# Kernel optimization log

Measured on AMD Instinct MI355X. Metric: run time of the kernel, lower is better.

The kernel has to match this reference:

```python
import jax, jax.numpy as jnp
import numpy as np
from jax import lax

B, T, S = 32, 64, 400
H, E, EMB, V = 512, 1024, 256, 32000


def setup_inputs() -> dict:
    key = jax.random.key(0)
    ks = jax.random.split(key, 16)
    w = lambda k, shape: jax.random.normal(k, shape, dtype=jnp.float32) * 0.05
    return {
        "target": jax.random.randint(ks[0], (B, T), 0, V),
        "h0": jax.random.normal(ks[1], (B, H), dtype=jnp.float32),
        "c0": jax.random.normal(ks[2], (B, H), dtype=jnp.float32),
        "enc_outs": jax.random.normal(ks[3], (S, B, E), dtype=jnp.float32),
        "attn_mask": jnp.ones((B, S), dtype=jnp.int32),
        "emb": w(ks[4], (V, EMB)),
        "W_ih": w(ks[5], (4 * H, EMB)),
        "b_ih": w(ks[6], (4 * H,)),
        "W_hh": w(ks[7], (4 * H, H)),
        "b_hh": w(ks[8], (4 * H,)),
        "W_attn": w(ks[9], (H, E)),
        "b_attn": w(ks[10], (H,)),
        "W_concat": w(ks[11], (H, E + H)),
        "b_concat": w(ks[12], (H,)),
        "W_out": w(ks[13], (V, H)),
        "b_out": w(ks[14], (V,)),
    }


def reference(target, h0, c0, enc_outs, attn_mask, emb, W_ih, b_ih, W_hh, b_hh,
              W_attn, b_attn, W_concat, b_concat, W_out, b_out):
    # Precompute attention keys projection once: [S, B, H]
    keys_proj = jnp.einsum("sbe,he->sbh", enc_outs, W_attn) + b_attn
    masked = attn_mask == 0  # [B, S]
    x_seq = emb[target].transpose(1, 0, 2)  # [T, B, EMB]

    def step(carry, x_t):
        h, c = carry
        # LSTMCell (torch gate order: i, f, g, o)
        gates = x_t @ W_ih.T + b_ih + h @ W_hh.T + b_hh  # [B, 4H]
        i, f, g, o = jnp.split(gates, 4, axis=1)
        c = jax.nn.sigmoid(f) * c + jax.nn.sigmoid(i) * jnp.tanh(g)
        h = jax.nn.sigmoid(o) * jnp.tanh(c)
        # additive-style attention: sum over hidden of query*key_proj
        scores = jnp.einsum("bh,sbh->bs", h, keys_proj)  # [B, S]
        scores = jnp.where(masked, jnp.float32(-1e18), scores)
        a = jax.nn.softmax(scores, axis=1)
        ctx = jnp.einsum("bs,sbe->be", a, enc_outs)  # [B, E]
        cat = jnp.tanh(jnp.concatenate([ctx, h], axis=1) @ W_concat.T + b_concat)
        logit = jax.nn.log_softmax(cat @ W_out.T + b_out, axis=-1)  # [B, V]
        return (h, c), logit

    (_, _), logits = lax.scan(step, (h0, c0), x_seq)  # [T, B, V]
    return logits.transpose(1, 0, 2)  # [B, T, V]
```

## Files before the change

### kernel.cpp

```cpp
#include <hip/hip_runtime.h>
#include <hip/hip_bf16.h>
#include <hip/hip_fp16.h>

#define B_ 32
#define T_ 64
#define S_ 400
#define SPAD_ 512
#define H_ 512
#define E_ 1024
#define EMB_ 256
#define V_ 32000

typedef _Float16 f16;
typedef _Float16 half8 __attribute__((ext_vector_type(8)));
typedef float f32x4 __attribute__((ext_vector_type(4)));
typedef float f32x16 __attribute__((ext_vector_type(16)));
typedef unsigned uint4v __attribute__((ext_vector_type(4)));

__device__ __forceinline__ void gl_lds16(const void* g, void* l) {
  __builtin_amdgcn_global_load_lds(
      (const __attribute__((address_space(1))) void*)g,
      (__attribute__((address_space(3))) void*)l, 16, 0, 0);
}

__device__ __forceinline__ float sigmoidf_(float x) { return 1.f / (1.f + expf(-x)); }

__device__ __forceinline__ uint4v load_b128_sys(const void* p) {
  uint4v r;
  asm volatile("global_load_dwordx4 %0, %1, off sc0 sc1" : "=v"(r) : "v"(p) : "memory");
  return r;
}
__device__ __forceinline__ void store_b128_sys(void* p, uint4v v) {
  asm volatile("global_store_dwordx4 %0, %1, off sc0 sc1" :: "v"(p), "v"(v) : "memory");
}

#define N2_ENC (S_ * B_ * E_ / 2)
#define N2_WA  (H_ * E_ / 2)
#define N2_WC  (H_ * (E_ + H_) / 2)
#define N2_WO  (V_ * H_ / 2)
#define N2_TOT (N2_ENC + N2_WA + N2_WC + N2_WO)
__global__ __launch_bounds__(256) void cvt_all_kernel(const float* __restrict__ enc,
                                                      const float* __restrict__ wa,
                                                      const float* __restrict__ wc,
                                                      const float* __restrict__ wo,
                                                      f16* __restrict__ enc_f,
                                                      f16* __restrict__ wa_f,
                                                      f16* __restrict__ wc_f,
                                                      f16* __restrict__ wo_f) {
  int i = blockIdx.x * 256 + threadIdx.x;
  if (i >= N2_TOT) return;
  const float* s; f16* d; int j;
  if (i < N2_ENC) { s = enc; d = enc_f; j = i; }
  else if (i < N2_ENC + N2_WA) { s = wa; d = wa_f; j = i - N2_ENC; }
  else if (i < N2_ENC + N2_WA + N2_WC) { s = wc; d = wc_f; j = i - N2_ENC - N2_WA; }
  else { s = wo; d = wo_f; j = i - N2_ENC - N2_WA - N2_WC; }
  float2 v = reinterpret_cast<const float2*>(s)[j];
  union { f16 h[2]; unsigned u; } o;
  o.h[0] = (f16)v.x; o.h[1] = (f16)v.y;
  reinterpret_cast<unsigned*>(d)[j] = o.u;
}

__global__ __launch_bounds__(256) void gather_x_kernel(const int* __restrict__ target,
                                                       const float* __restrict__ emb,
                                                       f16* __restrict__ xin) {
  int r = blockIdx.x;
  int t = r >> 5, b = r & 31;
  int tok = target[b * T_ + t];
  xin[(size_t)r * EMB_ + threadIdx.x] = (f16)emb[(size_t)tok * EMB_ + threadIdx.x];
}

__global__ __launch_bounds__(256) void prep_kernel(const float* __restrict__ b_ih,
                                                   const float* __restrict__ b_hh,
                                                   float* __restrict__ biasperm,
                                                   const float* __restrict__ Whh,
                                                   f16* __restrict__ Wperm,
                                                   const float* __restrict__ Wih,
                                                   f16* __restrict__ Wihp,
                                                   const float* __restrict__ h0,
                                                   f16* __restrict__ hbuf) {
  int idx = blockIdx.x * 256 + threadIdx.x;
  if (idx < 4 * H_) {
    int j = idx >> 2, gg = idx & 3;
    biasperm[idx] = b_ih[gg * H_ + j] + b_hh[gg * H_ + j];
  }
  if (idx < B_ * H_) hbuf[idx] = (f16)h0[idx];
  if (idx < T_ * B_ * H_ / 8) {
    uint4v p = {0xFFFFFFFFu, 0xFFFFFFFFu, 0xFFFFFFFFu, 0xFFFFFFFFu};
    reinterpret_cast<uint4v*>(reinterpret_cast<char*>(hbuf) + (size_t)B_ * H_ * 2)[idx] = p;
  }
  {
    int j = idx >> 9, k = idx & 511;
#pragma unroll
    for (int gg = 0; gg < 4; ++gg)
      Wperm[((size_t)(j * 4 + gg)) * H_ + k] = (f16)Whh[((size_t)(gg * H_ + j)) * H_ + k];
  }
  if (idx < H_ * EMB_) {
    int j = idx >> 8, k = idx & 255;
#pragma unroll
    for (int gg = 0; gg < 4; ++gg)
      Wihp[((size_t)(j * 4 + gg)) * EMB_ + k] = (f16)Wih[((size_t)(gg * H_ + j)) * EMB_ + k];
  }
}

template <int OUTK, bool DO_TANH>
__global__ __launch_bounds__(256) void gemm_bt_kernel(const f16* __restrict__ A,
                                                      const f16* __restrict__ W,
                                                      const float* __restrict__ bias,
                                                      void* __restrict__ outp,
                                                      int M, int N, int K) {
  __shared__ __align__(16) char As[128 * 64];
  __shared__ __align__(16) char Bs[128 * 64];
  const int tid = threadIdx.x;
  const int lane = tid & 63, wave = tid >> 6;
  const int wr = (wave >> 1) * 64, wc = (wave & 1) * 64;
  const int fr = lane & 15, fq = lane >> 4;
  const int row0 = blockIdx.x * 128, col0 = blockIdx.y * 128;

  f32x4 acc[4][4];
#pragma unroll
  for (int i = 0; i < 4; ++i)
#pragma unroll
    for (int j = 0; j < 4; ++j) acc[i][j] = {0.f, 0.f, 0.f, 0.f};

  for (int k0 = 0; k0 < K; k0 += 32) {
    __syncthreads();
#pragma unroll
    for (int i = 0; i < 2; ++i) {
      int o = tid * 16 + i * 4096;
      int r = o >> 6, kk = (o & 63) >> 1;
      gl_lds16(A + (size_t)(row0 + r) * K + (k0 + kk), As + o);
      gl_lds16(W + (size_t)(col0 + r) * K + (k0 + kk), Bs + o);
    }
    __syncthreads();
    half8 af[4], bfr[4];
#pragma unroll
    for (int mi = 0; mi < 4; ++mi)
      af[mi] = *reinterpret_cast<const half8*>(As + (wr + mi * 16 + fr) * 64 + fq * 16);
#pragma unroll
    for (int ni = 0; ni < 4; ++ni)
      bfr[ni] = *reinterpret_cast<const half8*>(Bs + (wc + ni * 16 + fr) * 64 + fq * 16);
#pragma unroll
    for (int mi = 0; mi < 4; ++mi)
#pragma unroll
      for (int ni = 0; ni < 4; ++ni)
        acc[mi][ni] = __builtin_amdgcn_mfma_f32_16x16x32_f16(af[mi], bfr[ni], acc[mi][ni], 0, 0, 0);
  }

#pragma unroll
  for (int mi = 0; mi < 4; ++mi)
#pragma unroll
    for (int ni = 0; ni < 4; ++ni)
#pragma unroll
      for (int r = 0; r < 4; ++r) {
        int row = row0 + wr + mi * 16 + fq * 4 + r;
        int col = col0 + wc + ni * 16 + fr;
        float v = acc[mi][ni][r] + bias[col];
        if (DO_TANH) v = tanhf(v);
        if (OUTK == 0) {
          ((float*)outp)[(size_t)row * N + col] = v;
        } else if (OUTK == 1) {
          ((f16*)outp)[(size_t)row * N + col] = (f16)v;
        } else {
          int orow = (row & 31) * T_ + (row >> 5);
          ((float*)outp)[(size_t)orow * N + col] = v;
        }
      }
}

__global__ __launch_bounds__(512, 1) void lstm_mfma_kernel(const float* __restrict__ xpart,
                                                           const f16* __restrict__ Wperm,
                                                           const float* __restrict__ c0,
                                                           f16* __restrict__ hbuf) {
  extern __shared__ char lds[];
  char* Abuf = lds;
  float* gates = (float*)(lds + 65536);
  unsigned* hstage = (unsigned*)(lds + 65536 + 33280);
  int* flags = (int*)(lds + 65536 + 33280 + 4096);

  const int g = blockIdx.x, tid = threadIdx.x;
  const int lane = tid & 63, wave = tid >> 6;
  const int ln31 = lane & 31, lh = lane >> 5;

  if (tid < 8) flags[tid] = 0;

  half8 wf[32];
  {
    const f16* wrow = Wperm + ((size_t)(g * 256 + wave * 32 + ln31)) * H_ + lh * 8;
#pragma unroll
    for (int kc = 0; kc < 32; ++kc)
      wf[kc] = *reinterpret_cast<const half8*>(wrow + kc * 16);
  }

  const int b = tid >> 4, qd = tid & 15;
  float cst[4];
#pragma unroll
  for (int jj = 0; jj < 4; ++jj)
    cst[jj] = c0[b * H_ + g * 64 + qd * 4 + jj];

  __syncthreads();

  for (int t = 0; t < T_; ++t) {
    const float* xr = xpart + ((size_t)(t * B_ + b)) * (4 * H_) + g * 256 + qd * 16;
    float4 xv[4];
#pragma unroll
    for (int i = 0; i < 4; ++i) xv[i] = *reinterpret_cast<const float4*>(xr + i * 4);

    {
      int p = (t == 0) ? wave : (wave + (wave >= g ? 1 : 0));
      bool duty = (t == 0) ? true : (wave < 7);
      if (duty) {
        const char* sb = (const char*)hbuf + (size_t)t * 32768 + ln31 * 1024 + p * 128 + lh * 16;
        while (true) {
          uint4v v0 = load_b128_sys(sb);
          uint4v v1 = load_b128_sys(sb + 32);
          uint4v v2 = load_b128_sys(sb + 64);
          uint4v v3 = load_b128_sys(sb + 96);
          asm volatile("s_waitcnt vmcnt(0)" ::: "memory");
          __builtin_amdgcn_sched_barrier(0);
          unsigned bad = 0;
#pragma unroll
          for (int d = 0; d < 4; ++d)
            bad |= (unsigned)(v0[d] == 0xFFFFFFFFu) | (unsigned)(v1[d] == 0xFFFFFFFFu) |
                   (unsigned)(v2[d] == 0xFFFFFFFFu) | (unsigned)(v3[d] == 0xFFFFFFFFu);
          if (__all(bad == 0)) {
            char* ab = Abuf + (size_t)(t & 1) * 32768 + lane * 16;
            *(uint4v*)(ab + (size_t)(4 * p + 0) * 1024) = v0;
            *(uint4v*)(ab + (size_t)(4 * p + 1) * 1024) = v1;
            *(uint4v*)(ab + (size_t)(4 * p + 2) * 1024) = v2;
            *(uint4v*)(ab + (size_t)(4 * p + 3) * 1024) = v3;
            asm volatile("s_waitcnt lgkmcnt(0)" ::: "memory");
            __builtin_amdgcn_sched_barrier(0);
            if (lane == 0)
              __hip_atomic_fetch_add(&flags[p], 1, __ATOMIC_RELAXED,
                                     __HIP_MEMORY_SCOPE_WORKGROUP);
            break;
          }
        }
      }
    }

    f32x16 acc;
#pragma unroll
    for (int r = 0; r < 16; ++r) acc[r] = 0.f;
    const char* abR = Abuf + (size_t)(t & 1) * 32768 + lane * 16;
    const char* hsR = (const char*)hstage + lane * 16;
    const int thr = t + 1;
#pragma unroll
    for (int ps = 0; ps < 8; ++ps) {
      if (ps == g && t > 0) {
#pragma unroll
        for (int c = 0; c < 4; ++c) {
          half8 a = *(const half8*)(hsR + c * 1024);
          acc = __builtin_amdgcn_mfma_f32_32x32x16_f16(a, wf[4 * ps + c], acc, 0, 0, 0);
        }
      } else {
        while (__hip_atomic_load(&flags[ps], __ATOMIC_ACQUIRE,
                                 __HIP_MEMORY_SCOPE_WORKGROUP) < thr) {}
#pragma unroll
        for (int c = 0; c < 4; ++c) {
          half8 a = *(const half8*)(abR + (size_t)(4 * ps + c) * 1024);
          acc = __builtin_amdgcn_mfma_f32_32x32x16_f16(a, wf[4 * ps + c], acc, 0, 0, 0);
        }
      }
    }
#pragma unroll
    for (int r = 0; r < 16; ++r) {
      int row = (r & 3) + 8 * (r >> 2) + 4 * lh;
      gates[row * 260 + wave * 32 + ln31] = acc[r];
    }
    __syncthreads();

    const float* gr = &gates[b * 260 + qd * 16];
    float hv[4];
#pragma unroll
    for (int jj = 0; jj < 4; ++jj) {
      float gi = gr[jj * 4 + 0] + xv[jj].x;
      float gf = gr[jj * 4 + 1] + xv[jj].y;
      float gg = gr[jj * 4 + 2] + xv[jj].z;
      float go = gr[jj * 4 + 3] + xv[jj].w;
      cst[jj] = sigmoidf_(gf) * cst[jj] + sigmoidf_(gi) * tanhf(gg);
      hv[jj] = sigmoidf_(go) * tanhf(cst[jj]);
    }
    union { f16 h[2]; unsigned u; } pk0, pk1;
    pk0.h[0] = (f16)hv[0]; pk0.h[1] = (f16)hv[1];
    pk1.h[0] = (f16)hv[2]; pk1.h[1] = (f16)hv[3];
    {
      int cp0 = 2 * qd, cp1 = 2 * qd + 1;
      hstage[((cp0 >> 3) * 64 + ((cp0 >> 2) & 1) * 32 + b) * 4 + (cp0 & 3)] = pk0.u;
      hstage[((cp1 >> 3) * 64 + ((cp1 >> 2) & 1) * 32 + b) * 4 + (cp1 & 3)] = pk1.u;
    }
    __syncthreads();

    if (tid < 256) {
      int kcl = tid >> 6, l2 = tid & 63;
      uint4v v = *(const uint4v*)((const char*)hstage + (kcl * 64 + l2) * 16);
      store_b128_sys((char*)hbuf + (size_t)(t + 1) * 32768 + (l2 & 31) * 1024 +
                         g * 128 + kcl * 32 + (l2 >> 5) * 16,
                     v);
    }
  }
}

__global__ __launch_bounds__(128) void catcopy_kernel(const f16* __restrict__ hseq,
                                                      f16* __restrict__ catin) {
  int r = blockIdx.x;
  const uint2* src = reinterpret_cast<const uint2*>(hseq + (size_t)r * H_);
  uint2* dst = reinterpret_cast<uint2*>(catin + (size_t)r * (E_ + H_) + E_);
  dst[threadIdx.x] = src[threadIdx.x];
}

__global__ __launch_bounds__(256) void scores_mfma_kernel(const f16* __restrict__ keys,
                                                          const f16* __restrict__ hseq,
                                                          float* __restrict__ attnw) {
  const int b = blockIdx.y;
  const int lane = threadIdx.x & 63, wave = threadIdx.x >> 6;
  const int ln31 = lane & 31, lh = lane >> 5;
  const int stile = blockIdx.x * 128 + wave * 32;
  const f16* ar  = keys + ((size_t)(stile + ln31) * B_ + b) * H_ + lh * 8;
  const f16* br0 = hseq + ((size_t)ln31 * B_ + b) * H_ + lh * 8;
  const f16* br1 = hseq + ((size_t)(ln31 + 32) * B_ + b) * H_ + lh * 8;
  f32x16 ac0, ac1;
#pragma unroll
  for (int r = 0; r < 16; ++r) { ac0[r] = 0.f; ac1[r] = 0.f; }
#pragma unroll
  for (int kc = 0; kc < 32; ++kc) {
    half8 a  = *reinterpret_cast<const half8*>(ar + kc * 16);
    half8 h0 = *reinterpret_cast<const half8*>(br0 + kc * 16);
    half8 h1 = *reinterpret_cast<const half8*>(br1 + kc * 16);
    ac0 = __builtin_amdgcn_mfma_f32_32x32x16_f16(a, h0, ac0, 0, 0, 0);
    ac1 = __builtin_amdgcn_mfma_f32_32x32x16_f16(a, h1, ac1, 0, 0, 0);
  }
#pragma unroll
  for (int r = 0; r < 16; ++r) {
    int s = stile + (r & 3) + 8 * (r >> 2) + 4 * lh;
    if (s < S_) {
      attnw[((size_t)b * S_ + s) * T_ + ln31]      = ac0[r];
      attnw[((size_t)b * S_ + s) * T_ + 32 + ln31] = ac1[r];
    }
  }
}

__global__ __launch_bounds__(64) void softmax_kernel(float* __restrict__ attnw,
                                                     const int* __restrict__ mask) {
  int b = blockIdx.x, t = blockIdx.y, l = threadIdx.x;
  float vals[7];
  float m = -3.4e38f;
#pragma unroll
  for (int i = 0; i < 7; ++i) {
    int s = l + i * 64;
    float v = -3.4e38f;
    if (s < S_) {
      v = attnw[((size_t)b * S_ + s) * T_ + t];
      if (mask[b * S_ + s] == 0) v = -1e18f;
    }
    vals[i] = v;
    m = fmaxf(m, v);
  }
#pragma unroll
  for (int o = 32; o > 0; o >>= 1) m = fmaxf(m, __shfl_xor(m, o));
  float sum = 0.f;
#pragma unroll
  for (int i = 0; i < 7; ++i) {
    int s = l + i * 64;
    if (s < S_) { float e = expf(vals[i] - m); vals[i] = e; sum += e; }
  }
#pragma unroll
  for (int o = 32; o > 0; o >>= 1) sum += __shfl_xor(sum, o);
  float inv = 1.f / sum;
#pragma unroll
  for (int i = 0; i < 7; ++i) {
    int s = l + i * 64;
    if (s < S_) attnw[((size_t)b * S_ + s) * T_ + t] = vals[i] * inv;
  }
}

__global__ __launch_bounds__(256) void ctx_kernel(const float* __restrict__ attnw,
                                                  const f16* __restrict__ enc,
                                                  f16* __restrict__ catin) {
  int b = blockIdx.x, e0 = blockIdx.y * 64;
  int el = threadIdx.x & 63, tq = threadIdx.x >> 6;
  __shared__ float a_lds[100 * 64];
  float acc[16];
#pragma unroll
  for (int i = 0; i < 16; ++i) acc[i] = 0.f;
  for (int sc = 0; sc < 4; ++sc) {
    __syncthreads();
    for (int i = threadIdx.x; i < 6400; i += 256)
      a_lds[i] = attnw[((size_t)b * S_ + sc * 100) * T_ + i];
    __syncthreads();
    for (int sl = 0; sl < 100; ++sl) {
      int s = sc * 100 + sl;
      float v = (float)enc[((size_t)s * B_ + b) * E_ + e0 + el];
#pragma unroll
      for (int i = 0; i < 16; ++i) acc[i] += a_lds[sl * 64 + tq * 16 + i] * v;
    }
  }
#pragma unroll
  for (int i = 0; i < 16; ++i) {
    int t = tq * 16 + i;
    catin[((size_t)t * B_ + b) * (E_ + H_) + e0 + el] = (f16)acc[i];
  }
}

__global__ __launch_bounds__(512, 1) void logsm_kernel(float* __restrict__ out) {
  int r = blockIdx.x;
  size_t base = (size_t)r * V_;
  int tid = threadIdx.x;
  float4* op = reinterpret_cast<float4*>(out + base);
  float4 v[16];
  float m = -3.4e38f;
#pragma unroll
  for (int k = 0; k < 16; ++k) {
    int c = tid + (k << 9);
    if (c < 8000) {
      v[k] = op[c];
      m = fmaxf(m, fmaxf(fmaxf(v[k].x, v[k].y), fmaxf(v[k].z, v[k].w)));
    }
  }
  __shared__ float red[8];
#pragma unroll
  for (int o = 32; o > 0; o >>= 1) m = fmaxf(m, __shfl_xor(m, o));
  if ((tid & 63) == 0) red[tid >> 6] = m;
  __syncthreads();
  float mm = red[0];
#pragma unroll
  for (int i = 1; i < 8; ++i) mm = fmaxf(mm, red[i]);
  float s = 0.f;
#pragma unroll
  for (int k = 0; k < 16; ++k) {
    int c = tid + (k << 9);
    if (c < 8000)
      s += expf(v[k].x - mm) + expf(v[k].y - mm) + expf(v[k].z - mm) + expf(v[k].w - mm);
  }
#pragma unroll
  for (int o = 32; o > 0; o >>= 1) s += __shfl_xor(s, o);
  __syncthreads();
  if ((tid & 63) == 0) red[tid >> 6] = s;
  __syncthreads();
  s = 0.f;
#pragma unroll
  for (int i = 0; i < 8; ++i) s += red[i];
  float lse = mm + logf(s);
#pragma unroll
  for (int k = 0; k < 16; ++k) {
    int c = tid + (k << 9);
    if (c < 8000) {
      float4 o4;
      o4.x = v[k].x - lse; o4.y = v[k].y - lse;
      o4.z = v[k].z - lse; o4.w = v[k].w - lse;
      op[c] = o4;
    }
  }
}

extern "C" void kernel_launch(void* const* d_in, const int* in_sizes, int n_in,
                              void* d_out, int out_size, void* d_ws, size_t ws_size,
                              hipStream_t stream) {
  const int*   target = (const int*)d_in[0];
  const float* h0     = (const float*)d_in[1];
  const float* c0     = (const float*)d_in[2];
  const float* enc    = (const float*)d_in[3];
  const int*   mask   = (const int*)d_in[4];
  const float* emb    = (const float*)d_in[5];
  const float* W_ih   = (const float*)d_in[6];
  const float* b_ih   = (const float*)d_in[7];
  const float* W_hh   = (const float*)d_in[8];
  const float* b_hh   = (const float*)d_in[9];
  const float* W_attn = (const float*)d_in[10];
  const float* b_attn = (const float*)d_in[11];
  const float* W_cat  = (const float*)d_in[12];
  const float* b_cat  = (const float*)d_in[13];
  const float* W_out  = (const float*)d_in[14];
  const float* b_out  = (const float*)d_in[15];

  char* ws = (char*)d_ws;
  size_t off = 0;
  auto alloc = [&](size_t bytes) {
    void* p = ws + off;
    off = (off + bytes + 255) & ~(size_t)255;
    return p;
  };
  f16*   enc_f    = (f16*)alloc((size_t)S_ * B_ * E_ * 2);
  f16*   keys_f   = (f16*)alloc((size_t)SPAD_ * B_ * H_ * 2);
  f16*   Wattn_f  = (f16*)alloc((size_t)H_ * E_ * 2);
  f16*   Wcat_f   = (f16*)alloc((size_t)H_ * (E_ + H_) * 2);
  f16*   Wout_f   = (f16*)alloc((size_t)V_ * H_ * 2);
  f16*   Wperm    = (f16*)alloc((size_t)4 * H_ * H_ * 2);
  f16*   Wihp     = (f16*)alloc((size_t)4 * H_ * EMB_ * 2);
  float* biasperm = (float*)alloc((size_t)4 * H_ * 4);
  f16*   xin_f    = (f16*)alloc((size_t)T_ * B_ * EMB_ * 2);
  float* xpart    = (float*)alloc((size_t)T_ * B_ * 4 * H_ * 4);
  f16*   catin_f  = (f16*)alloc((size_t)T_ * B_ * (E_ + H_) * 2);
  float* attnw    = (float*)alloc((size_t)B_ * S_ * T_ * 4);
  f16*   catbuf_f = (f16*)alloc((size_t)T_ * B_ * H_ * 2);
  f16*   hbuf     = (f16*)alloc((size_t)(T_ + 1) * B_ * H_ * 2);
  (void)ws_size; (void)in_sizes; (void)n_in; (void)out_size;

  f16* hseq_f = hbuf + (size_t)B_ * H_;

  cvt_all_kernel<<<(N2_TOT + 255) / 256, 256, 0, stream>>>(
      enc, W_attn, W_cat, W_out, enc_f, Wattn_f, Wcat_f, Wout_f);
  gather_x_kernel<<<T_ * B_, 256, 0, stream>>>(target, emb, xin_f);
  prep_kernel<<<(H_ * H_) / 256, 256, 0, stream>>>(b_ih, b_hh, biasperm, W_hh, Wperm,
                                                   W_ih, Wihp, h0, hbuf);

  gemm_bt_kernel<1, false><<<dim3((S_ * B_) / 128, H_ / 128), 256, 0, stream>>>(
      enc_f, Wattn_f, b_attn, keys_f, S_ * B_, H_, E_);
  gemm_bt_kernel<0, false><<<dim3((T_ * B_) / 128, (4 * H_) / 128), 256, 0, stream>>>(
      xin_f, Wihp, biasperm, xpart, T_ * B_, 4 * H_, EMB_);

  lstm_mfma_kernel<<<8, 512, 65536 + 33280 + 4096 + 32, stream>>>(xpart, Wperm, c0, hbuf);

  catcopy_kernel<<<T_ * B_, 128, 0, stream>>>(hseq_f, catin_f);
  scores_mfma_kernel<<<dim3(SPAD_ / 128, B_), 256, 0, stream>>>(keys_f, hseq_f, attnw);
  softmax_kernel<<<dim3(B_, T_), 64, 0, stream>>>(attnw, mask);
  ctx_kernel<<<dim3(B_, E_ / 64), 256, 0, stream>>>(attnw, enc_f, catin_f);

  gemm_bt_kernel<1, true><<<dim3((T_ * B_) / 128, H_ / 128), 256, 0, stream>>>(
      catin_f, Wcat_f, b_cat, catbuf_f, T_ * B_, H_, E_ + H_);
  gemm_bt_kernel<2, false><<<dim3((T_ * B_) / 128, V_ / 128), 256, 0, stream>>>(
      catbuf_f, Wout_f, b_out, (float*)d_out, T_ * B_, V_, H_);

  logsm_kernel<<<B_ * T_, 512, 0, stream>>>((float*)d_out);
}
```

Before: 791.0 us.

## Overlap LSTM recurrence with keys GEMM and weight casts; fuse log-softmax partials

Merges the serial 8-block LSTM kernel with the keys-projection GEMM (which now converts fp32 encoder rows inline) and the fp16 conversion of W_concat/W_out into one mega kernel. The other CUs, idle during the recurrence, can then do this work in parallel. The standalone encoder fp16 copy is dropped and ctx reads fp32 enc directly. The output GEMM now writes fp16 logits with per-64-column max/sum partials, followed by an LSE combine and a final subtract pass, replacing the full fp32 log-softmax reread. Risks: keys blocks may compete with the latency-critical LSTM blocks for bandwidth, and the fp16 logit store loses precision.

New measurement: 745.2 us. -5.8%, faster.

```diff
diff --git a/kernel.cpp b/kernel.cpp
--- a/kernel.cpp
+++ b/kernel.cpp
@@ -10,6 +10,12 @@
 #define E_ 1024
 #define EMB_ 256
 #define V_ 32000
+#define NCB_ 500
+
+#define KEYS_BLOCKS 200
+#define CVT_BLOCKS 48
+#define MEGA_BLOCKS (8 + KEYS_BLOCKS + CVT_BLOCKS)
+#define MEGA_LDS (65536 + 33280 + 4096 + 32)
 
 typedef _Float16 f16;
 typedef _Float16 half8 __attribute__((ext_vector_type(8)));
@@ -32,32 +38,6 @@
 }
 __device__ __forceinline__ void store_b128_sys(void* p, uint4v v) {
   asm volatile("global_store_dwordx4 %0, %1, off sc0 sc1" :: "v"(p), "v"(v) : "memory");
-}
-
-#define N2_ENC (S_ * B_ * E_ / 2)
-#define N2_WA  (H_ * E_ / 2)
-#define N2_WC  (H_ * (E_ + H_) / 2)
-#define N2_WO  (V_ * H_ / 2)
-#define N2_TOT (N2_ENC + N2_WA + N2_WC + N2_WO)
-__global__ __launch_bounds__(256) void cvt_all_kernel(const float* __restrict__ enc,
-                                                      const float* __restrict__ wa,
-                                                      const float* __restrict__ wc,
-                                                      const float* __restrict__ wo,
-                                                      f16* __restrict__ enc_f,
-                                                      f16* __restrict__ wa_f,
-                                                      f16* __restrict__ wc_f,
-                                                      f16* __restrict__ wo_f) {
-  int i = blockIdx.x * 256 + threadIdx.x;
-  if (i >= N2_TOT) return;
-  const float* s; f16* d; int j;
-  if (i < N2_ENC) { s = enc; d = enc_f; j = i; }
-  else if (i < N2_ENC + N2_WA) { s = wa; d = wa_f; j = i - N2_ENC; }
-  else if (i < N2_ENC + N2_WA + N2_WC) { s = wc; d = wc_f; j = i - N2_ENC - N2_WA; }
-  else { s = wo; d = wo_f; j = i - N2_ENC - N2_WA - N2_WC; }
-  float2 v = reinterpret_cast<const float2*>(s)[j];
-  union { f16 h[2]; unsigned u; } o;
-  o.h[0] = (f16)v.x; o.h[1] = (f16)v.y;
-  reinterpret_cast<unsigned*>(d)[j] = o.u;
 }
 
 __global__ __launch_bounds__(256) void gather_x_kernel(const int* __restrict__ target,
@@ -77,7 +57,9 @@
                                                    const float* __restrict__ Wih,
                                                    f16* __restrict__ Wihp,
                                                    const float* __restrict__ h0,
-                                                   f16* __restrict__ hbuf) {
+                                                   f16* __restrict__ hbuf,
+                                                   const float* __restrict__ Wattn,
+                                                   f16* __restrict__ Wattn_f) {
   int idx = blockIdx.x * 256 + threadIdx.x;
   if (idx < 4 * H_) {
     int j = idx >> 2, gg = idx & 3;
@@ -99,6 +81,12 @@
 #pragma unroll
     for (int gg = 0; gg < 4; ++gg)
       Wihp[((size_t)(j * 4 + gg)) * EMB_ + k] = (f16)Wih[((size_t)(gg * H_ + j)) * EMB_ + k];
+  }
+  {
+    float2 v = reinterpret_cast<const float2*>(Wattn)[idx];
+    union { f16 h[2]; unsigned u; } o;
+    o.h[0] = (f16)v.x; o.h[1] = (f16)v.y;
+    reinterpret_cast<unsigned*>(Wattn_f)[idx] = o.u;
   }
 }
 
@@ -167,136 +155,217 @@
       }
 }
 
-__global__ __launch_bounds__(512, 1) void lstm_mfma_kernel(const float* __restrict__ xpart,
-                                                           const f16* __restrict__ Wperm,
-                                                           const float* __restrict__ c0,
-                                                           f16* __restrict__ hbuf) {
+__global__ __launch_bounds__(512, 1) void mega_kernel(
+    const float* __restrict__ xpart, const f16* __restrict__ Wperm,
+    const float* __restrict__ c0, f16* __restrict__ hbuf,
+    const float* __restrict__ enc, const f16* __restrict__ Wattn_f,
+    const float* __restrict__ b_attn, f16* __restrict__ keys,
+    const float* __restrict__ wc_src, f16* __restrict__ wc_dst,
+    const float* __restrict__ wo_src, f16* __restrict__ wo_dst) {
   extern __shared__ char lds[];
-  char* Abuf = lds;
-  float* gates = (float*)(lds + 65536);
-  unsigned* hstage = (unsigned*)(lds + 65536 + 33280);
-  int* flags = (int*)(lds + 65536 + 33280 + 4096);
-
-  const int g = blockIdx.x, tid = threadIdx.x;
+  const int blk = blockIdx.x, tid = threadIdx.x;
   const int lane = tid & 63, wave = tid >> 6;
-  const int ln31 = lane & 31, lh = lane >> 5;
-
-  if (tid < 8) flags[tid] = 0;
-
-  half8 wf[32];
-  {
-    const f16* wrow = Wperm + ((size_t)(g * 256 + wave * 32 + ln31)) * H_ + lh * 8;
-#pragma unroll
-    for (int kc = 0; kc < 32; ++kc)
-      wf[kc] = *reinterpret_cast<const half8*>(wrow + kc * 16);
-  }
-
-  const int b = tid >> 4, qd = tid & 15;
-  float cst[4];
-#pragma unroll
-  for (int jj = 0; jj < 4; ++jj)
-    cst[jj] = c0[b * H_ + g * 64 + qd * 4 + jj];
-
-  __syncthreads();
-
-  for (int t = 0; t < T_; ++t) {
-    const float* xr = xpart + ((size_t)(t * B_ + b)) * (4 * H_) + g * 256 + qd * 16;
-    float4 xv[4];
-#pragma unroll
-    for (int i = 0; i < 4; ++i) xv[i] = *reinterpret_cast<const float4*>(xr + i * 4);
-
+
+  if (blk < 8) {
+    char* Abuf = lds;
+    float* gates = (float*)(lds + 65536);
+    unsigned* hstage = (unsigned*)(lds + 65536 + 33280);
+    int* flags = (int*)(lds + 65536 + 33280 + 4096);
+    const int g = blk;
+    const int ln31 = lane & 31, lh = lane >> 5;
+
+    if (tid < 8) flags[tid] = 0;
+
+    half8 wf[32];
     {
-      int p = (t == 0) ? wave : (wave + (wave >= g ? 1 : 0));
-      bool duty = (t == 0) ? true : (wave < 7);
-      if (duty) {
-        const char* sb = (const char*)hbuf + (size_t)t * 32768 + ln31 * 1024 + p * 128 + lh * 16;
-        while (true) {
-          uint4v v0 = load_b128_sys(sb);
-          uint4v v1 = load_b128_sys(sb + 32);
-          uint4v v2 = load_b128_sys(sb + 64);
-          uint4v v3 = load_b128_sys(sb + 96);
-          asm volatile("s_waitcnt vmcnt(0)" ::: "memory");
-          __builtin_amdgcn_sched_barrier(0);
-          unsigned bad = 0;
-#pragma unroll
-          for (int d = 0; d < 4; ++d)
-            bad |= (unsigned)(v0[d] == 0xFFFFFFFFu) | (unsigned)(v1[d] == 0xFFFFFFFFu) |
-                   (unsigned)(v2[d] == 0xFFFFFFFFu) | (unsigned)(v3[d] == 0xFFFFFFFFu);
-          if (__all(bad == 0)) {
-            char* ab = Abuf + (size_t)(t & 1) * 32768 + lane * 16;
-            *(uint4v*)(ab + (size_t)(4 * p + 0) * 1024) = v0;
-            *(uint4v*)(ab + (size_t)(4 * p + 1) * 1024) = v1;
-            *(uint4v*)(ab + (size_t)(4 * p + 2) * 1024) = v2;
-            *(uint4v*)(ab + (size_t)(4 * p + 3) * 1024) = v3;
-            asm volatile("s_waitcnt lgkmcnt(0)" ::: "memory");
+      const f16* wrow = Wperm + ((size_t)(g * 256 + wave * 32 + ln31)) * H_ + lh * 8;
+#pragma unroll
+      for (int kc = 0; kc < 32; ++kc)
+        wf[kc] = *reinterpret_cast<const half8*>(wrow + kc * 16);
+    }
+
+    const int b = tid >> 4, qd = tid & 15;
+    float cst[4];
+#pragma unroll
+    for (int jj = 0; jj < 4; ++jj)
+      cst[jj] = c0[b * H_ + g * 64 + qd * 4 + jj];
+
+    __syncthreads();
+
+    for (int t = 0; t < T_; ++t) {
+      const float* xr = xpart + ((size_t)(t * B_ + b)) * (4 * H_) + g * 256 + qd * 16;
+      float4 xv[4];
+#pragma unroll
+      for (int i = 0; i < 4; ++i) xv[i] = *reinterpret_cast<const float4*>(xr + i * 4);
+
+      {
+        int p = (t == 0) ? wave : (wave + (wave >= g ? 1 : 0));
+        bool duty = (t == 0) ? true : (wave < 7);
+        if (duty) {
+          const char* sb = (const char*)hbuf + (size_t)t * 32768 + ln31 * 1024 + p * 128 + lh * 16;
+          while (true) {
+            uint4v v0 = load_b128_sys(sb);
+            uint4v v1 = load_b128_sys(sb + 32);
+            uint4v v2 = load_b128_sys(sb + 64);
+            uint4v v3 = load_b128_sys(sb + 96);
+            asm volatile("s_waitcnt vmcnt(0)" ::: "memory");
             __builtin_amdgcn_sched_barrier(0);
-            if (lane == 0)
-              __hip_atomic_fetch_add(&flags[p], 1, __ATOMIC_RELAXED,
-                                     __HIP_MEMORY_SCOPE_WORKGROUP);
-            break;
+            unsigned bad = 0;
+#pragma unroll
+            for (int d = 0; d < 4; ++d)
+              bad |= (unsigned)(v0[d] == 0xFFFFFFFFu) | (unsigned)(v1[d] == 0xFFFFFFFFu) |
+                     (unsigned)(v2[d] == 0xFFFFFFFFu) | (unsigned)(v3[d] == 0xFFFFFFFFu);
+            if (__all(bad == 0)) {
+              char* ab = Abuf + (size_t)(t & 1) * 32768 + lane * 16;
+              *(uint4v*)(ab + (size_t)(4 * p + 0) * 1024) = v0;
+              *(uint4v*)(ab + (size_t)(4 * p + 1) * 1024) = v1;
+              *(uint4v*)(ab + (size_t)(4 * p + 2) * 1024) = v2;
+              *(uint4v*)(ab + (size_t)(4 * p + 3) * 1024) = v3;
+              asm volatile("s_waitcnt lgkmcnt(0)" ::: "memory");
+              __builtin_amdgcn_sched_barrier(0);
+              if (lane == 0)
+                __hip_atomic_fetch_add(&flags[p], 1, __ATOMIC_RELAXED,
+                                       __HIP_MEMORY_SCOPE_WORKGROUP);
+              break;
+            }
           }
         }
       }
-    }
-
-    f32x16 acc;
-#pragma unroll
-    for (int r = 0; r < 16; ++r) acc[r] = 0.f;
-    const char* abR = Abuf + (size_t)(t & 1) * 32768 + lane * 16;
-    const char* hsR = (const char*)hstage + lane * 16;
-    const int thr = t + 1;
-#pragma unroll
-    for (int ps = 0; ps < 8; ++ps) {
-      if (ps == g && t > 0) {
-#pragma unroll
-        for (int c = 0; c < 4; ++c) {
-          half8 a = *(const half8*)(hsR + c * 1024);
-          acc = __builtin_amdgcn_mfma_f32_32x32x16_f16(a, wf[4 * ps + c], acc, 0, 0, 0);
+
+      f32x16 acc;
+#pragma unroll
+      for (int r = 0; r < 16; ++r) acc[r] = 0.f;
+      const char* abR = Abuf + (size_t)(t & 1) * 32768 + lane * 16;
+      const char* hsR = (const char*)hstage + lane * 16;
+      const int thr = t + 1;
+#pragma unroll
+      for (int ps = 0; ps < 8; ++ps) {
+        if (ps == g && t > 0) {
+#pragma unroll
+          for (int c = 0; c < 4; ++c) {
+            half8 a = *(const half8*)(hsR + c * 1024);
+            acc = __builtin_amdgcn_mfma_f32_32x32x16_f16(a, wf[4 * ps + c], acc, 0, 0, 0);
+          }
+        } else {
+          while (__hip_atomic_load(&flags[ps], __ATOMIC_ACQUIRE,
+                                   __HIP_MEMORY_SCOPE_WORKGROUP) < thr) {}
+#pragma unroll
+          for (int c = 0; c < 4; ++c) {
+            half8 a = *(const half8*)(abR + (size_t)(4 * ps + c) * 1024);
+            acc = __builtin_amdgcn_mfma_f32_32x32x16_f16(a, wf[4 * ps + c], acc, 0, 0, 0);
+          }
         }
-      } else {
-        while (__hip_atomic_load(&flags[ps], __ATOMIC_ACQUIRE,
-                                 __HIP_MEMORY_SCOPE_WORKGROUP) < thr) {}
-#pragma unroll
-        for (int c = 0; c < 4; ++c) {
-          half8 a = *(const half8*)(abR + (size_t)(4 * ps + c) * 1024);
-          acc = __builtin_amdgcn_mfma_f32_32x32x16_f16(a, wf[4 * ps + c], acc, 0, 0, 0);
+      }
+      const int ln31b = lane & 31, lhb = lane >> 5;
+#pragma unroll
+      for (int r = 0; r < 16; ++r) {
+        int row = (r & 3) + 8 * (r >> 2) + 4 * lhb;
+        gates[row * 260 + wave * 32 + ln31b] = acc[r];
+      }
+      __syncthreads();
+
+      const float* gr = &gates[b * 260 + qd * 16];
+      float hv[4];
+#pragma unroll
+      for (int jj = 0; jj < 4; ++jj) {
+        float gi = gr[jj * 4 + 0] + xv[jj].x;
+        float gf = gr[jj * 4 + 1] + xv[jj].y;
+        float gg = gr[jj * 4 + 2] + xv[jj].z;
+        float go = gr[jj * 4 + 3] + xv[jj].w;
+        cst[jj] = sigmoidf_(gf) * cst[jj] + sigmoidf_(gi) * tanhf(gg);
+        hv[jj] = sigmoidf_(go) * tanhf(cst[jj]);
+      }
+      union { f16 h[2]; unsigned u; } pk0, pk1;
+      pk0.h[0] = (f16)hv[0]; pk0.h[1] = (f16)hv[1];
+      pk1.h[0] = (f16)hv[2]; pk1.h[1] = (f16)hv[3];
+      {
+        int cp0 = 2 * qd, cp1 = 2 * qd + 1;
+        hstage[((cp0 >> 3) * 64 + ((cp0 >> 2) & 1) * 32 + b) * 4 + (cp0 & 3)] = pk0.u;
+        hstage[((cp1 >> 3) * 64 + ((cp1 >> 2) & 1) * 32 + b) * 4 + (cp1 & 3)] = pk1.u;
+      }
+      __syncthreads();
+
+      if (tid < 256) {
+        int kcl = tid >> 6, l2 = tid & 63;
+        uint4v v = *(const uint4v*)((const char*)hstage + (kcl * 64 + l2) * 16);
+        store_b128_sys((char*)hbuf + (size_t)(t + 1) * 32768 + (l2 & 31) * 1024 +
+                           g * 128 + kcl * 32 + (l2 >> 5) * 16,
+                       v);
+      }
+    }
+  } else if (blk < 8 + KEYS_BLOCKS) {
+    char* As = lds;
+    char* Bs = lds + 16384;
+    const int kid = blk - 8;
+    const int row0 = (kid % 50) * 256, col0 = (kid / 50) * 128;
+    const int wr = (wave >> 1) * 64, wc = (wave & 1) * 64;
+    const int fr = lane & 15, fq = lane >> 4;
+
+    f32x4 acc[4][4];
+#pragma unroll
+    for (int i = 0; i < 4; ++i)
+#pragma unroll
+      for (int j = 0; j < 4; ++j) acc[i][j] = {0.f, 0.f, 0.f, 0.f};
+
+    for (int k0 = 0; k0 < E_; k0 += 32) {
+      __syncthreads();
+      float4 av[4];
+#pragma unroll
+      for (int i = 0; i < 4; ++i) {
+        int idx = tid + i * 512;
+        int r = idx >> 3, ck = (idx & 7) * 4;
+        av[i] = *reinterpret_cast<const float4*>(enc + (size_t)(row0 + r) * E_ + k0 + ck);
+      }
+      {
+        int o = tid * 16;
+        int r = o >> 6, kk = (o & 63) >> 1;
+        gl_lds16(Wattn_f + (size_t)(col0 + r) * E_ + (k0 + kk), Bs + o);
+      }
+#pragma unroll
+      for (int i = 0; i < 4; ++i) {
+        int idx = tid + i * 512;
+        int r = idx >> 3, ck = (idx & 7) * 4;
+        union { f16 h[4]; unsigned long long u; } p;
+        p.h[0] = (f16)av[i].x; p.h[1] = (f16)av[i].y;
+        p.h[2] = (f16)av[i].z; p.h[3] = (f16)av[i].w;
+        *reinterpret_cast<unsigned long long*>(As + r * 64 + ck * 2) = p.u;
+      }
+      __syncthreads();
+      half8 af[4], bf[4];
+#pragma unroll
+      for (int mi = 0; mi < 4; ++mi)
+        af[mi] = *reinterpret_cast<const half8*>(As + (wr + mi * 16 + fr) * 64 + fq * 16);
+#pragma unroll
+      for (int ni = 0; ni < 4; ++ni)
+        bf[ni] = *reinterpret_cast<const half8*>(Bs + (wc + ni * 16 + fr) * 64 + fq * 16);
+#pragma unroll
+      for (int mi = 0; mi < 4; ++mi)
+#pragma unroll
+        for (int ni = 0; ni < 4; ++ni)
+          acc[mi][ni] = __builtin_amdgcn_mfma_f32_16x16x32_f16(af[mi], bf[ni], acc[mi][ni], 0, 0, 0);
+    }
+#pragma unroll
+    for (int mi = 0; mi < 4; ++mi)
+#pragma unroll
+      for (int ni = 0; ni < 4; ++ni)
+#pragma unroll
+        for (int r = 0; r < 4; ++r) {
+          int row = row0 + wr + mi * 16 + fq * 4 + r;
+          int col = col0 + wc + ni * 16 + fr;
+          keys[(size_t)row * H_ + col] = (f16)(acc[mi][ni][r] + b_attn[col]);
         }
-      }
-    }
-#pragma unroll
-    for (int r = 0; r < 16; ++r) {
-      int row = (r & 3) + 8 * (r >> 2) + 4 * lh;
-      gates[row * 260 + wave * 32 + ln31] = acc[r];
-    }
-    __syncthreads();
-
-    const float* gr = &gates[b * 260 + qd * 16];
-    float hv[4];
-#pragma unroll
-    for (int jj = 0; jj < 4; ++jj) {
-      float gi = gr[jj * 4 + 0] + xv[jj].x;
-      float gf = gr[jj * 4 + 1] + xv[jj].y;
-      float gg = gr[jj * 4 + 2] + xv[jj].z;
-      float go = gr[jj * 4 + 3] + xv[jj].w;
-      cst[jj] = sigmoidf_(gf) * cst[jj] + sigmoidf_(gi) * tanhf(gg);
-      hv[jj] = sigmoidf_(go) * tanhf(cst[jj]);
-    }
-    union { f16 h[2]; unsigned u; } pk0, pk1;
-    pk0.h[0] = (f16)hv[0]; pk0.h[1] = (f16)hv[1];
-    pk1.h[0] = (f16)hv[2]; pk1.h[1] = (f16)hv[3];
-    {
-      int cp0 = 2 * qd, cp1 = 2 * qd + 1;
-      hstage[((cp0 >> 3) * 64 + ((cp0 >> 2) & 1) * 32 + b) * 4 + (cp0 & 3)] = pk0.u;
-      hstage[((cp1 >> 3) * 64 + ((cp1 >> 2) & 1) * 32 + b) * 4 + (cp1 & 3)] = pk1.u;
-    }
-    __syncthreads();
-
-    if (tid < 256) {
-      int kcl = tid >> 6, l2 = tid & 63;
-      uint4v v = *(const uint4v*)((const char*)hstage + (kcl * 64 + l2) * 16);
-      store_b128_sys((char*)hbuf + (size_t)(t + 1) * 32768 + (l2 & 31) * 1024 +
-                         g * 128 + kcl * 32 + (l2 >> 5) * 16,
-                     v);
+  } else {
+    const int N2WC = H_ * (E_ + H_) / 2, N2WO = V_ * H_ / 2;
+    const int total = N2WC + N2WO;
+    const int stride = CVT_BLOCKS * 512;
+    for (int i = (blk - 8 - KEYS_BLOCKS) * 512 + tid; i < total; i += stride) {
+      const float* s; f16* d; int j;
+      if (i < N2WC) { s = wc_src; d = wc_dst; j = i; }
+      else { s = wo_src; d = wo_dst; j = i - N2WC; }
+      float2 v = reinterpret_cast<const float2*>(s)[j];
+      union { f16 h[2]; unsigned u; } o;
+      o.h[0] = (f16)v.x; o.h[1] = (f16)v.y;
+      reinterpret_cast<unsigned*>(d)[j] = o.u;
     }
   }
 }
@@ -375,7 +444,7 @@
 }
 
 __global__ __launch_bounds__(256) void ctx_kernel(const float* __restrict__ attnw,
-                                                  const f16* __restrict__ enc,
+                                                  const float* __restrict__ enc,
                                                   f16* __restrict__ catin) {
   int b = blockIdx.x, e0 = blockIdx.y * 64;
   int el = threadIdx.x & 63, tq = threadIdx.x >> 6;
@@ -390,7 +459,7 @@
     __syncthreads();
     for (int sl = 0; sl < 100; ++sl) {
       int s = sc * 100 + sl;
-      float v = (float)enc[((size_t)s * B_ + b) * E_ + e0 + el];
+      float v = enc[((size_t)s * B_ + b) * E_ + e0 + el];
 #pragma unroll
       for (int i = 0; i < 16; ++i) acc[i] += a_lds[sl * 64 + tq * 16 + i] * v;
     }
@@ -399,6 +468,120 @@
   for (int i = 0; i < 16; ++i) {
     int t = tq * 16 + i;
     catin[((size_t)t * B_ + b) * (E_ + H_) + e0 + el] = (f16)acc[i];
+  }
+}
+
+__global__ __launch_bounds__(256) void gemm_out_kernel(const f16* __restrict__ A,
+                                                       const f16* __restrict__ W,
+                                                       const float* __restrict__ bias,
+                                                       f16* __restrict__ lbuf,
+                                                       float* __restrict__ pm,
+                                                       float* __restrict__ ps) {
+  __shared__ __align__(16) char As[128 * 64];
+  __shared__ __align__(16) char Bs[128 * 64];
+  const int tid = threadIdx.x;
+  const int lane = tid & 63, wave = tid >> 6;
+  const int wr = (wave >> 1) * 64, wc = (wave & 1) * 64;
+  const int fr = lane & 15, fq = lane >> 4;
+  const int row0 = blockIdx.x * 128, col0 = blockIdx.y * 128;
+
+  f32x4 acc[4][4];
+#pragma unroll
+  for (int i = 0; i < 4; ++i)
+#pragma unroll
+    for (int j = 0; j < 4; ++j) acc[i][j] = {0.f, 0.f, 0.f, 0.f};
+
+  for (int k0 = 0; k0 < H_; k0 += 32) {
+    __syncthreads();
+#pragma unroll
+    for (int i = 0; i < 2; ++i) {
+      int o = tid * 16 + i * 4096;
+      int r = o >> 6, kk = (o & 63) >> 1;
+      gl_lds16(A + (size_t)(row0 + r) * H_ + (k0 + kk), As + o);
+      gl_lds16(W + (size_t)(col0 + r) * H_ + (k0 + kk), Bs + o);
+    }
+    __syncthreads();
+    half8 af[4], bfr[4];
+#pragma unroll
+    for (int mi = 0; mi < 4; ++mi)
+      af[mi] = *reinterpret_cast<const half8*>(As + (wr + mi * 16 + fr) * 64 + fq * 16);
+#pragma unroll
+    for (int ni = 0; ni < 4; ++ni)
+      bfr[ni] = *reinterpret_cast<const half8*>(Bs + (wc + ni * 16 + fr) * 64 + fq * 16);
+#pragma unroll
+    for (int mi = 0; mi < 4; ++mi)
+#pragma unroll
+      for (int ni = 0; ni < 4; ++ni)
+        acc[mi][ni] = __builtin_amdgcn_mfma_f32_16x16x32_f16(af[mi], bfr[ni], acc[mi][ni], 0, 0, 0);
+  }
+
+#pragma unroll
+  for (int mi = 0; mi < 4; ++mi)
+#pragma unroll
+    for (int r = 0; r < 4; ++r) {
+      int row = row0 + wr + mi * 16 + fq * 4 + r;
+      float v0 = acc[mi][0][r] + bias[col0 + wc + fr];
+      float v1 = acc[mi][1][r] + bias[col0 + wc + 16 + fr];
+      float v2 = acc[mi][2][r] + bias[col0 + wc + 32 + fr];
+      float v3 = acc[mi][3][r] + bias[col0 + wc + 48 + fr];
+      f16* lp = lbuf + (size_t)row * V_ + col0 + wc + fr;
+      lp[0] = (f16)v0; lp[16] = (f16)v1; lp[32] = (f16)v2; lp[48] = (f16)v3;
+      float mx = fmaxf(fmaxf(v0, v1), fmaxf(v2, v3));
+#pragma unroll
+      for (int d2 = 1; d2 <= 8; d2 <<= 1) mx = fmaxf(mx, __shfl_xor(mx, d2));
+      float sm = expf(v0 - mx) + expf(v1 - mx) + expf(v2 - mx) + expf(v3 - mx);
+#pragma unroll
+      for (int d2 = 1; d2 <= 8; d2 <<= 1) sm += __shfl_xor(sm, d2);
+      if (fr == 0) {
+        int cb = (col0 + wc) >> 6;
+        pm[(size_t)row * NCB_ + cb] = mx;
+        ps[(size_t)row * NCB_ + cb] = sm;
+      }
+    }
+}
+
+__global__ __launch_bounds__(64) void lse_combine_kernel(const float* __restrict__ pm,
+                                                         const float* __restrict__ ps,
+                                                         float* __restrict__ lse) {
+  int row = blockIdx.x, l = threadIdx.x;
+  float mv[8], sv[8];
+  float m = -3.4e38f;
+#pragma unroll
+  for (int i = 0; i < 8; ++i) {
+    int idx = l + i * 64;
+    if (idx < NCB_) {
+      mv[i] = pm[(size_t)row * NCB_ + idx];
+      sv[i] = ps[(size_t)row * NCB_ + idx];
+    } else { mv[i] = -3.4e38f; sv[i] = 0.f; }
+    m = fmaxf(m, mv[i]);
+  }
+#pragma unroll
+  for (int o = 32; o > 0; o >>= 1) m = fmaxf(m, __shfl_xor(m, o));
+  float s = 0.f;
+#pragma unroll
+  for (int i = 0; i < 8; ++i) s += sv[i] * expf(mv[i] - m);
+#pragma unroll
+  for (int o = 32; o > 0; o >>= 1) s += __shfl_xor(s, o);
+  if (l == 0) lse[row] = m + logf(s);
+}
+
+__global__ __launch_bounds__(256) void final_out_kernel(const f16* __restrict__ lbuf,
+                                                        const float* __restrict__ lse,
+                                                        float* __restrict__ out) {
+  int j = blockIdx.x;
+  int b = j >> 6, t = j & 63;
+  int r = t * B_ + b;
+  float l = lse[r];
+  const half8* src = reinterpret_cast<const half8*>(lbuf + (size_t)r * V_);
+  float4* dst = reinterpret_cast<float4*>(out + (size_t)j * V_);
+  for (int c = threadIdx.x; c < V_ / 8; c += 256) {
+    half8 h = src[c];
+    float4 o1, o2;
+    o1.x = (float)h[0] - l; o1.y = (float)h[1] - l;
+    o1.z = (float)h[2] - l; o1.w = (float)h[3] - l;
+    o2.x = (float)h[4] - l; o2.y = (float)h[5] - l;
+    o2.z = (float)h[6] - l; o2.w = (float)h[7] - l;
+    dst[c * 2] = o1; dst[c * 2 + 1] = o2;
   }
 }
 
@@ -480,7 +663,6 @@
     off = (off + bytes + 255) & ~(size_t)255;
     return p;
   };
-  f16*   enc_f    = (f16*)alloc((size_t)S_ * B_ * E_ * 2);
   f16*   keys_f   = (f16*)alloc((size_t)SPAD_ * B_ * H_ * 2);
   f16*   Wattn_f  = (f16*)alloc((size_t)H_ * E_ * 2);
   f16*   Wcat_f   = (f16*)alloc((size_t)H_ * (E_ + H_) * 2);
@@ -494,32 +676,47 @@
   float* attnw    = (float*)alloc((size_t)B_ * S_ * T_ * 4);
   f16*   catbuf_f = (f16*)alloc((size_t)T_ * B_ * H_ * 2);
   f16*   hbuf     = (f16*)alloc((size_t)(T_ + 1) * B_ * H_ * 2);
-  (void)ws_size; (void)in_sizes; (void)n_in; (void)out_size;
+
+  size_t extra = ((size_t)T_ * B_ * V_ * 2 + 255 + (size_t)T_ * B_ * NCB_ * 4 * 2 + 512 +
+                  (size_t)T_ * B_ * 4 + 256);
+  bool pathA = (off + extra) <= ws_size;
+  f16* lbuf = nullptr; float* pm = nullptr; float* psb = nullptr; float* lse = nullptr;
+  if (pathA) {
+    lbuf = (f16*)alloc((size_t)T_ * B_ * V_ * 2);
+    pm   = (float*)alloc((size_t)T_ * B_ * NCB_ * 4);
+    psb  = (float*)alloc((size_t)T_ * B_ * NCB_ * 4);
+    lse  = (float*)alloc((size_t)T_ * B_ * 4);
+  }
+  (void)in_sizes; (void)n_in; (void)out_size;
 
   f16* hseq_f = hbuf + (size_t)B_ * H_;
 
-  cvt_all_kernel<<<(N2_TOT + 255) / 256, 256, 0, stream>>>(
-      enc, W_attn, W_cat, W_out, enc_f, Wattn_f, Wcat_f, Wout_f);
   gather_x_kernel<<<T_ * B_, 256, 0, stream>>>(target, emb, xin_f);
   prep_kernel<<<(H_ * H_) / 256, 256, 0, stream>>>(b_ih, b_hh, biasperm, W_hh, Wperm,
-                                                   W_ih, Wihp, h0, hbuf);
-
-  gemm_bt_kernel<1, false><<<dim3((S_ * B_) / 128, H_ / 128), 256, 0, stream>>>(
-      enc_f, Wattn_f, b_attn, keys_f, S_ * B_, H_, E_);
+                                                   W_ih, Wihp, h0, hbuf, W_attn, Wattn_f);
   gemm_bt_kernel<0, false><<<dim3((T_ * B_) / 128, (4 * H_) / 128), 256, 0, stream>>>(
       xin_f, Wihp, biasperm, xpart, T_ * B_, 4 * H_, EMB_);
 
-  lstm_mfma_kernel<<<8, 512, 65536 + 33280 + 4096 + 32, stream>>>(xpart, Wperm, c0, hbuf);
+  mega_kernel<<<MEGA_BLOCKS, 512, MEGA_LDS, stream>>>(
+      xpart, Wperm, c0, hbuf, enc, Wattn_f, b_attn, keys_f,
+      W_cat, Wcat_f, W_out, Wout_f);
 
   catcopy_kernel<<<T_ * B_, 128, 0, stream>>>(hseq_f, catin_f);
   scores_mfma_kernel<<<dim3(SPAD_ / 128, B_), 256, 0, stream>>>(keys_f, hseq_f, attnw);
   softmax_kernel<<<dim3(B_, T_), 64, 0, stream>>>(attnw, mask);
-  ctx_kernel<<<dim3(B_, E_ / 64), 256, 0, stream>>>(attnw, enc_f, catin_f);
+  ctx_kernel<<<dim3(B_, E_ / 64), 256, 0, stream>>>(attnw, enc, catin_f);
 
   gemm_bt_kernel<1, true><<<dim3((T_ * B_) / 128, H_ / 128), 256, 0, stream>>>(
       catin_f, Wcat_f, b_cat, catbuf_f, T_ * B_, H_, E_ + H_);
-  gemm_bt_kernel<2, false><<<dim3((T_ * B_) / 128, V_ / 128), 256, 0, stream>>>(
-      catbuf_f, Wout_f, b_out, (float*)d_out, T_ * B_, V_, H_);
-
-  logsm_kernel<<<B_ * T_, 512, 0, stream>>>((float*)d_out);
-}
+
+  if (pathA) {
+    gemm_out_kernel<<<dim3((T_ * B_) / 128, V_ / 128), 256, 0, stream>>>(
+        catbuf_f, Wout_f, b_out, lbuf, pm, psb);
+    lse_combine_kernel<<<T_ * B_, 64, 0, stream>>>(pm, psb, lse);
+    final_out_kernel<<<T_ * B_, 256, 0, stream>>>(lbuf, lse, (float*)d_out);
+  } else {
+    gemm_bt_kernel<2, false><<<dim3((T_ * B_) / 128, V_ / 128), 256, 0, stream>>>(
+        catbuf_f, Wout_f, b_out, (float*)d_out, T_ * B_, V_, H_);
+    logsm_kernel<<<B_ * T_, 512, 0, stream>>>((float*)d_out);
+  }
+}
```
